# Kernel tuning notes

Hardware: AMD Instinct MI355X
Metric: run time of the kernel (lower is better)

Reference implementation:

```python
import jax, jax.numpy as jnp
import numpy as np

E = 512      # embed_dim
H = 8        # num_heads
D = E // H   # head_dim = 64
R = 32       # rot_dims (partial rotary)
THETA = 10000.0


def _rope(x):
    # x: [B, H, S, D]; rotate first R dims (interleaved pairs, lucidrains-style)
    S = x.shape[-2]
    inv_freq = THETA ** (-jnp.arange(0, R, 2, dtype=jnp.float32) / R)  # [R/2]
    ang = jnp.arange(S, dtype=jnp.float32)[:, None] * inv_freq          # [S, R/2]
    c, s = jnp.cos(ang), jnp.sin(ang)
    xr, xp = x[..., :R], x[..., R:]
    x1, x2 = xr[..., 0::2], xr[..., 1::2]
    rot = jnp.stack([x1 * c - x2 * s, x1 * s + x2 * c], axis=-1).reshape(xr.shape)
    return jnp.concatenate([rot, xp], axis=-1)


def setup_inputs() -> dict:
    key = jax.random.key(0)
    k1, k2, k3, k4 = jax.random.split(key, 4)
    B, S = 4, 2048
    x = jax.random.normal(k1, (B, S, E), dtype=jnp.float32)
    input_mask = jax.random.randint(k2, (B, S), 0, 2).astype(bool)
    W_in = jax.random.normal(k3, (3 * E, E), dtype=jnp.float32) / np.sqrt(E).astype(np.float32)
    W_out = jax.random.normal(k4, (E, E), dtype=jnp.float32) / np.sqrt(E).astype(np.float32)
    return {"x": x, "input_mask": input_mask, "W_in": W_in, "W_out": W_out}


def reference(x, input_mask, W_in, W_out):
    B, S, _ = x.shape
    # fused QKV projection (Linear, no bias): x @ W_in.T -> [B,S,3E]
    qkv = (x @ W_in.T).reshape(B, S, 3, H, D).transpose(2, 0, 3, 1, 4)  # [3,B,H,S,D]
    q, k, v = qkv[0], qkv[1], qkv[2]
    q = _rope(q)
    k = _rope(k)
    # mask: causal AND (both tokens valid OR diagonal)
    causal = jnp.tril(jnp.ones((S, S), dtype=bool))
    inv = ~input_mask                                  # [B,S]
    cross = inv[:, None, :] | inv[:, :, None]          # [B,S,S]
    square = (~cross) | jnp.eye(S, dtype=bool)         # diagonal forced True
    full = causal[None, :, :] & square                 # [B,S,S]
    scores = jnp.einsum('bhsd,bhtd->bhst', q, k) / np.float32(np.sqrt(D))
    scores = jnp.where(full[:, None, :, :], scores, -jnp.inf)
    probs = jax.nn.softmax(scores, axis=-1)
    attn = jnp.einsum('bhst,bhtd->bhsd', probs, v)
    attn = attn.transpose(0, 2, 1, 3).reshape(B, S, E)
    return attn @ W_out.T
```

## Files before the change

kernel.cpp:

```cpp
#include <hip/hip_runtime.h>
#include <math.h>

#define B_ 4
#define S_ 2048
#define E_ 512
#define H_ 8
#define D_ 64

typedef short bf16x8 __attribute__((ext_vector_type(8)));
typedef float f32x4 __attribute__((ext_vector_type(4)));

__device__ inline short f2bf(float f) {
  union { float f; unsigned u; } v; v.f = f;
  unsigned r = v.u + 0x7FFF + ((v.u >> 16) & 1);
  return (short)(r >> 16);
}
__device__ inline short f2bf_fast(float f) {
  union { float f; unsigned u; } v; v.f = f;
  return (short)((v.u + 0x8000u) >> 16);
}
__device__ inline float bf2f(short s) {
  union { unsigned u; float f; } v; v.u = ((unsigned)(unsigned short)s) << 16;
  return v.f;
}

__global__ __launch_bounds__(256) void cvt_all(
    const float* __restrict__ x, const float* __restrict__ win,
    const float* __restrict__ wout, short* __restrict__ xb,
    short* __restrict__ winb, short* __restrict__ woutb) {
  int bid = blockIdx.x;
  const float* src; short* dst; int i;
  if (bid < 4096)      { src = x;    dst = xb;    i = bid * 256 + threadIdx.x; }
  else if (bid < 4864) { src = win;  dst = winb;  i = (bid - 4096) * 256 + threadIdx.x; }
  else                 { src = wout; dst = woutb; i = (bid - 4864) * 256 + threadIdx.x; }
  float4 f = ((const float4*)src)[i];
  short4 o;
  o.x = f2bf(f.x); o.y = f2bf(f.y); o.z = f2bf(f.z); o.w = f2bf(f.w);
  ((short4*)dst)[i] = o;
}

__global__ __launch_bounds__(256) void gemm_qkv_mfma(
    const short* __restrict__ Xb,
    const short* __restrict__ Wb,
    short* __restrict__ qb, short* __restrict__ kb, short* __restrict__ vbT) {
  __shared__ __align__(16) short As[128][40];
  __shared__ __align__(16) short Bs[64][40];
  const int tid = threadIdx.x;
  const int w = tid >> 6, lane = tid & 63;
  const int l15 = lane & 15, quad = lane >> 4;
  const int wm = w & 1, wn = w >> 1;
  const int m0 = blockIdx.x * 128;
  const int n0 = blockIdx.y * 64;
  f32x4 acc[4][2];
  for (int mt = 0; mt < 4; ++mt)
    for (int nt = 0; nt < 2; ++nt) acc[mt][nt] = (f32x4){0.f, 0.f, 0.f, 0.f};

  for (int k0 = 0; k0 < E_; k0 += 32) {
    __syncthreads();
    for (int l = 0; l < 2; ++l) {
      int c = tid + 256 * l;
      int row = c >> 2, k8 = (c & 3) * 8;
      *(bf16x8*)&As[row][k8] = *(const bf16x8*)&Xb[(size_t)(m0 + row) * E_ + k0 + k8];
    }
    {
      int row = tid >> 2, k8 = (tid & 3) * 8;
      *(bf16x8*)&Bs[row][k8] = *(const bf16x8*)&Wb[(size_t)(n0 + row) * E_ + k0 + k8];
    }
    __syncthreads();
    bf16x8 a[4], bfr[2];
    for (int mt = 0; mt < 4; ++mt)
      a[mt] = *(const bf16x8*)&As[wm * 64 + mt * 16 + l15][quad * 8];
    for (int nt = 0; nt < 2; ++nt)
      bfr[nt] = *(const bf16x8*)&Bs[wn * 32 + nt * 16 + l15][quad * 8];
    for (int mt = 0; mt < 4; ++mt)
      for (int nt = 0; nt < 2; ++nt)
        acc[mt][nt] = __builtin_amdgcn_mfma_f32_16x16x32_bf16(a[mt], bfr[nt], acc[mt][nt], 0, 0, 0);
  }
  const int t3 = n0 >> 9;
  for (int nt = 0; nt < 2; ++nt) {
    const int n = n0 + wn * 32 + nt * 16 + l15;
    const int h = (n >> 6) & 7;
    const int d = n & 63;
    const bool dorope = (t3 < 2) && (d < 32);
    const float sgn = (d & 1) ? 1.f : -1.f;
    const float fr = dorope ? powf(10000.f, -(float)(2 * (d >> 1)) * (1.f / 32.f)) : 0.f;
    for (int mt = 0; mt < 4; ++mt) {
      for (int i = 0; i < 4; ++i) {
        const int m = m0 + wm * 64 + mt * 16 + quad * 4 + i;
        const int b = m >> 11, s = m & (S_ - 1);
        float val = acc[mt][nt][i];
        float pv = __shfl_xor(val, 1, 64);
        float outv = val;
        if (dorope) {
          float ang = (float)s * fr;
          float sn, cs;
          sincosf(ang, &sn, &cs);
          outv = val * cs + pv * sgn * sn;
        }
        if (t3 == 2)
          vbT[((size_t)(b * 8 + h) * D_ + d) * S_ + s] = f2bf(outv);
        else {
          short* dst = (t3 == 0) ? qb : kb;
          dst[(((size_t)(b * 8 + h)) * S_ + s) * D_ + d] = f2bf(outv);
        }
      }
    }
  }
}

__global__ __launch_bounds__(256) void gemm_out_mfma(
    const short* __restrict__ Ab, const short* __restrict__ Wb,
    float* __restrict__ out) {
  __shared__ __align__(16) short As[128][40];
  __shared__ __align__(16) short Bs[64][40];
  const int tid = threadIdx.x;
  const int w = tid >> 6, lane = tid & 63;
  const int l15 = lane & 15, quad = lane >> 4;
  const int wm = w & 1, wn = w >> 1;
  const int m0 = blockIdx.x * 128;
  const int n0 = blockIdx.y * 64;
  f32x4 acc[4][2];
  for (int mt = 0; mt < 4; ++mt)
    for (int nt = 0; nt < 2; ++nt) acc[mt][nt] = (f32x4){0.f, 0.f, 0.f, 0.f};

  for (int k0 = 0; k0 < E_; k0 += 32) {
    __syncthreads();
    for (int l = 0; l < 2; ++l) {
      int c = tid + 256 * l;
      int row = c >> 2, k8 = (c & 3) * 8;
      *(bf16x8*)&As[row][k8] = *(const bf16x8*)&Ab[(size_t)(m0 + row) * E_ + k0 + k8];
    }
    {
      int row = tid >> 2, k8 = (tid & 3) * 8;
      *(bf16x8*)&Bs[row][k8] = *(const bf16x8*)&Wb[(size_t)(n0 + row) * E_ + k0 + k8];
    }
    __syncthreads();
    bf16x8 a[4], bfr[2];
    for (int mt = 0; mt < 4; ++mt)
      a[mt] = *(const bf16x8*)&As[wm * 64 + mt * 16 + l15][quad * 8];
    for (int nt = 0; nt < 2; ++nt)
      bfr[nt] = *(const bf16x8*)&Bs[wn * 32 + nt * 16 + l15][quad * 8];
    for (int mt = 0; mt < 4; ++mt)
      for (int nt = 0; nt < 2; ++nt)
        acc[mt][nt] = __builtin_amdgcn_mfma_f32_16x16x32_bf16(a[mt], bfr[nt], acc[mt][nt], 0, 0, 0);
  }
  for (int mt = 0; mt < 4; ++mt)
    for (int nt = 0; nt < 2; ++nt) {
      const int n = n0 + wn * 32 + nt * 16 + l15;
      for (int i = 0; i < 4; ++i) {
        const int m = m0 + wm * 64 + mt * 16 + quad * 4 + i;
        out[(size_t)m * E_ + n] = acc[mt][nt][i];
      }
    }
}

__global__ __launch_bounds__(256) void flash_mfma(
    const short* __restrict__ qb, const short* __restrict__ kb,
    const short* __restrict__ vbT, const int* __restrict__ maskp,
    short* __restrict__ pb0, short* __restrict__ pb1,
    float* __restrict__ lb0, float* __restrict__ lb1,
    short* __restrict__ ob) {
  __shared__ __align__(16) short Ks[64][72];
  __shared__ __align__(16) short VT[64][72];
  __shared__ __align__(16) short Pl[4][16][72];
  __shared__ float kbias[64];
  const int tid = threadIdx.x;
  const int w = tid >> 6, lane = tid & 63;
  const int l15 = lane & 15, quad = lane >> 4;
  const int bid = blockIdx.x;
  const int u = bid & 7, v = bid >> 3;
  const int bh = (u << 2) | (v & 3);
  const int w2 = v >> 2;
  const int pair = w2 & 15;
  const int kh = w2 >> 4;
  const int b = bh >> 3, hd = bh & 7;
  const short* qbase = qb + (size_t)bh * S_ * D_;
  const short* kbase = kb + (size_t)bh * S_ * D_;
  const short* vtb   = vbT + (size_t)bh * D_ * S_;
  short* PB = kh ? pb1 : pb0;
  float* LB = kh ? lb1 : lb0;
  const float c2 = 0.1803368801f;
  bf16x8 ones;
  for (int j = 0; j < 8; ++j) ones[j] = (short)0x3F80;

  for (int seg = 0; seg < 2; ++seg) {
    const int qt = (seg == 0) ? pair : 31 - pair;
    const int r0 = qt * 64;
    const int mid = (qt + 2) >> 1;
    const int lo = kh ? mid : 0;
    const int hi = kh ? (qt + 1) : mid;
    bf16x8 aq[2];
    {
      const short* qrow = qbase + (size_t)(r0 + 16 * w + l15) * D_;
      aq[0] = *(const bf16x8*)&qrow[quad * 8];
      aq[1] = *(const bf16x8*)&qrow[32 + quad * 8];
    }
    f32x4 o[4], lsum;
    for (int no = 0; no < 4; ++no) o[no] = (f32x4){0.f, 0.f, 0.f, 0.f};
    lsum = (f32x4){0.f, 0.f, 0.f, 0.f};

    for (int kt = lo; kt < hi; ++kt) {
      const int t0 = kt * 64;
      __syncthreads();
      for (int l = 0; l < 2; ++l) {
        int idx = tid + 256 * l;
        int row = idx >> 3, ch = (idx & 7) * 8;
        *(bf16x8*)&Ks[row][ch] = *(const bf16x8*)(kbase + (size_t)(t0 + row) * D_ + ch);
        *(bf16x8*)&VT[row][ch] = *(const bf16x8*)(vtb + (size_t)row * S_ + t0 + ch);
      }
      if (tid < 64)
        kbias[tid] = maskp[b * S_ + t0 + tid] ? -23.08312f : -1.0e38f;
      __syncthreads();
      f32x4 sfr[4];
      for (int nb = 0; nb < 4; ++nb) sfr[nb] = (f32x4){0.f, 0.f, 0.f, 0.f};
      for (int nb = 0; nb < 4; ++nb)
        for (int ks = 0; ks < 2; ++ks) {
          bf16x8 bk = *(const bf16x8*)&Ks[l15 + 16 * nb][32 * ks + quad * 8];
          sfr[nb] = __builtin_amdgcn_mfma_f32_16x16x32_bf16(aq[ks], bk, sfr[nb], 0, 0, 0);
        }
      if (kt < qt) {
        for (int nb = 0; nb < 4; ++nb) {
          const float bb = kbias[l15 + 16 * nb];
          for (int i = 0; i < 4; ++i)
            Pl[w][quad * 4 + i][l15 + 16 * nb] = f2bf_fast(exp2f(sfr[nb][i] * c2 + bb));
        }
      } else {
        for (int nb = 0; nb < 4; ++nb) {
          const int tg = l15 + 16 * nb;
          const float bb = kbias[l15 + 16 * nb];
          for (int i = 0; i < 4; ++i) {
            const float bbi = (tg > 16 * w + quad * 4 + i) ? -1.0e38f : bb;
            Pl[w][quad * 4 + i][l15 + 16 * nb] = f2bf_fast(exp2f(sfr[nb][i] * c2 + bbi));
          }
        }
      }
      asm volatile("s_waitcnt lgkmcnt(0)" ::: "memory");
      bf16x8 ap0 = *(const bf16x8*)&Pl[w][l15][quad * 8];
      bf16x8 ap1 = *(const bf16x8*)&Pl[w][l15][32 + quad * 8];
      for (int no = 0; no < 4; ++no) {
        bf16x8 bv0 = *(const bf16x8*)&VT[16 * no + l15][quad * 8];
        bf16x8 bv1 = *(const bf16x8*)&VT[16 * no + l15][32 + quad * 8];
        o[no] = __builtin_amdgcn_mfma_f32_16x16x32_bf16(ap0, bv0, o[no], 0, 0, 0);
        o[no] = __builtin_amdgcn_mfma_f32_16x16x32_bf16(ap1, bv1, o[no], 0, 0, 0);
      }
      lsum = __builtin_amdgcn_mfma_f32_16x16x32_bf16(ap0, ones, lsum, 0, 0, 0);
      lsum = __builtin_amdgcn_mfma_f32_16x16x32_bf16(ap1, ones, lsum, 0, 0, 0);
    }
    for (int i = 0; i < 4; ++i) {
      const int s = r0 + 16 * w + quad * 4 + i;
      const int qm = maskp[b * S_ + s];
      const size_t row = (size_t)(b * S_ + s) * E_ + hd * D_;
      if (kh == 0 && !qm) {
        for (int no = 0; no < 4; ++no) {
          const int d = l15 + 16 * no;
          ob[row + d] = vtb[(size_t)d * S_ + s];
        }
      }
      for (int no = 0; no < 4; ++no)
        PB[row + l15 + 16 * no] = f2bf(o[no][i]);
      if (l15 == 0)
        LB[bh * S_ + s] = lsum[i];
    }
  }
}

__global__ __launch_bounds__(256) void merge_kernel(
    const short* __restrict__ pb0, const short* __restrict__ pb1,
    const float* __restrict__ lb0, const float* __restrict__ lb1,
    const int* __restrict__ maskp, short* __restrict__ ob) {
  int idx = blockIdx.x * 256 + threadIdx.x;
  int m = idx >> 6, e = (idx & 63) * 8;
  if (!maskp[m]) return;
  int b = m >> 11, s = m & (S_ - 1);
  int bh = b * 8 + (e >> 6);
  float l = lb0[bh * S_ + s] + lb1[bh * S_ + s];
  float inv = 1.f / l;
  bf16x8 p0 = *(const bf16x8*)&pb0[(size_t)m * E_ + e];
  bf16x8 p1 = *(const bf16x8*)&pb1[(size_t)m * E_ + e];
  bf16x8 r;
  for (int j = 0; j < 8; ++j)
    r[j] = f2bf((bf2f(p0[j]) + bf2f(p1[j])) * inv);
  *(bf16x8*)&ob[(size_t)m * E_ + e] = r;
}

extern "C" void kernel_launch(void* const* d_in, const int* in_sizes, int n_in,
                              void* d_out, int out_size, void* d_ws, size_t ws_size,
                              hipStream_t stream) {
  const float* x    = (const float*)d_in[0];
  const int*   mask = (const int*)d_in[1];
  const float* Win  = (const float*)d_in[2];
  const float* Wout = (const float*)d_in[3];
  float* out = (float*)d_out;

  short* Xb    = (short*)d_ws;
  short* Winb  = Xb + 8192 * 512;
  short* Woutb = Winb + 1536 * 512;
  short* qb    = Woutb + 512 * 512;
  short* kb    = qb + 32 * 2048 * 64;
  short* vbT   = kb + 32 * 2048 * 64;
  short* ob    = vbT + 32 * 2048 * 64;
  short* pb0   = ob + 8192 * 512;
  short* pb1   = pb0 + 8192 * 512;
  float* lb0   = (float*)(pb1 + 8192 * 512);
  float* lb1   = lb0 + 32 * 2048;

  cvt_all<<<5120, 256, 0, stream>>>(x, Win, Wout, Xb, Winb, Woutb);
  gemm_qkv_mfma<<<dim3(64, 24), 256, 0, stream>>>(Xb, Winb, qb, kb, vbT);
  flash_mfma<<<1024, 256, 0, stream>>>(qb, kb, vbT, mask, pb0, pb1, lb0, lb1, ob);
  merge_kernel<<<2048, 256, 0, stream>>>(pb0, pb1, lb0, lb1, mask, ob);
  gemm_out_mfma<<<dim3(64, 8), 256, 0, stream>>>(ob, Woutb, out);
}
```

Measured before the change: 169.9 us.

## Use direct global-to-LDS loads and 128x128 tiles in QKV GEMM

Both projection GEMMs now stage their A and B tiles with global_load_lds. This writes global data straight into shared memory instead of passing it through registers, and it drops the padded LDS layout. The QKV GEMM also widens its N tile from 64 to 128, so each wave holds a 4x4 MFMA accumulator grid and the grid has half as many blocks. The RoPE frequency now comes from exp2f instead of powf. Removing the row padding may add LDS bank conflicts on fragment reads, and the larger tile raises register pressure.

```diff
diff --git a/kernel.cpp b/kernel.cpp
--- a/kernel.cpp
+++ b/kernel.cpp
@@ -22,6 +22,12 @@
 __device__ inline float bf2f(short s) {
   union { unsigned u; float f; } v; v.u = ((unsigned)(unsigned short)s) << 16;
   return v.f;
+}
+
+__device__ __forceinline__ void gload16(const short* g, short* l) {
+  __builtin_amdgcn_global_load_lds(
+      (__attribute__((address_space(1))) void*)g,
+      (__attribute__((address_space(3))) void*)l, 16, 0, 0);
 }
 
 __global__ __launch_bounds__(256) void cvt_all(
@@ -43,47 +49,59 @@
     const short* __restrict__ Xb,
     const short* __restrict__ Wb,
     short* __restrict__ qb, short* __restrict__ kb, short* __restrict__ vbT) {
-  __shared__ __align__(16) short As[128][40];
-  __shared__ __align__(16) short Bs[64][40];
+  __shared__ __align__(16) short As[128 * 32];
+  __shared__ __align__(16) short Bs[128 * 32];
   const int tid = threadIdx.x;
   const int w = tid >> 6, lane = tid & 63;
   const int l15 = lane & 15, quad = lane >> 4;
   const int wm = w & 1, wn = w >> 1;
   const int m0 = blockIdx.x * 128;
-  const int n0 = blockIdx.y * 64;
-  f32x4 acc[4][2];
+  const int n0 = blockIdx.y * 128;
+
+  const int srow = tid >> 2, sch = (tid & 3) * 8;
+  const short* gA0 = Xb + (size_t)(m0 + srow) * E_ + sch;
+  const short* gA1 = Xb + (size_t)(m0 + srow + 64) * E_ + sch;
+  const short* gB0 = Wb + (size_t)(n0 + srow) * E_ + sch;
+  const short* gB1 = Wb + (size_t)(n0 + srow + 64) * E_ + sch;
+  short* lA0 = &As[tid * 8];
+  short* lA1 = &As[tid * 8 + 2048];
+  short* lB0 = &Bs[tid * 8];
+  short* lB1 = &Bs[tid * 8 + 2048];
+
+  f32x4 acc[4][4];
   for (int mt = 0; mt < 4; ++mt)
-    for (int nt = 0; nt < 2; ++nt) acc[mt][nt] = (f32x4){0.f, 0.f, 0.f, 0.f};
+    for (int nt = 0; nt < 4; ++nt) acc[mt][nt] = (f32x4){0.f, 0.f, 0.f, 0.f};
 
   for (int k0 = 0; k0 < E_; k0 += 32) {
     __syncthreads();
-    for (int l = 0; l < 2; ++l) {
-      int c = tid + 256 * l;
-      int row = c >> 2, k8 = (c & 3) * 8;
-      *(bf16x8*)&As[row][k8] = *(const bf16x8*)&Xb[(size_t)(m0 + row) * E_ + k0 + k8];
-    }
-    {
-      int row = tid >> 2, k8 = (tid & 3) * 8;
-      *(bf16x8*)&Bs[row][k8] = *(const bf16x8*)&Wb[(size_t)(n0 + row) * E_ + k0 + k8];
-    }
+    gload16(gA0, lA0);
+    gload16(gA1, lA1);
+    gload16(gB0, lB0);
+    gload16(gB1, lB1);
+    gA0 += 32; gA1 += 32; gB0 += 32; gB1 += 32;
     __syncthreads();
-    bf16x8 a[4], bfr[2];
+    bf16x8 a[4], bfr[4];
+#pragma unroll
     for (int mt = 0; mt < 4; ++mt)
-      a[mt] = *(const bf16x8*)&As[wm * 64 + mt * 16 + l15][quad * 8];
-    for (int nt = 0; nt < 2; ++nt)
-      bfr[nt] = *(const bf16x8*)&Bs[wn * 32 + nt * 16 + l15][quad * 8];
+      a[mt] = *(const bf16x8*)&As[(wm * 64 + mt * 16 + l15) * 32 + quad * 8];
+#pragma unroll
+    for (int nt = 0; nt < 4; ++nt)
+      bfr[nt] = *(const bf16x8*)&Bs[(wn * 64 + nt * 16 + l15) * 32 + quad * 8];
+#pragma unroll
     for (int mt = 0; mt < 4; ++mt)
-      for (int nt = 0; nt < 2; ++nt)
+#pragma unroll
+      for (int nt = 0; nt < 4; ++nt)
         acc[mt][nt] = __builtin_amdgcn_mfma_f32_16x16x32_bf16(a[mt], bfr[nt], acc[mt][nt], 0, 0, 0);
   }
+
   const int t3 = n0 >> 9;
-  for (int nt = 0; nt < 2; ++nt) {
-    const int n = n0 + wn * 32 + nt * 16 + l15;
+  for (int nt = 0; nt < 4; ++nt) {
+    const int n = n0 + wn * 64 + nt * 16 + l15;
     const int h = (n >> 6) & 7;
     const int d = n & 63;
     const bool dorope = (t3 < 2) && (d < 32);
     const float sgn = (d & 1) ? 1.f : -1.f;
-    const float fr = dorope ? powf(10000.f, -(float)(2 * (d >> 1)) * (1.f / 32.f)) : 0.f;
+    const float fr = dorope ? exp2f((float)(d >> 1) * -0.8304820237f) : 0.f;
     for (int mt = 0; mt < 4; ++mt) {
       for (int i = 0; i < 4; ++i) {
         const int m = m0 + wm * 64 + mt * 16 + quad * 4 + i;
@@ -111,36 +129,44 @@
 __global__ __launch_bounds__(256) void gemm_out_mfma(
     const short* __restrict__ Ab, const short* __restrict__ Wb,
     float* __restrict__ out) {
-  __shared__ __align__(16) short As[128][40];
-  __shared__ __align__(16) short Bs[64][40];
+  __shared__ __align__(16) short As[128 * 32];
+  __shared__ __align__(16) short Bs[64 * 32];
   const int tid = threadIdx.x;
   const int w = tid >> 6, lane = tid & 63;
   const int l15 = lane & 15, quad = lane >> 4;
   const int wm = w & 1, wn = w >> 1;
   const int m0 = blockIdx.x * 128;
   const int n0 = blockIdx.y * 64;
+
+  const int srow = tid >> 2, sch = (tid & 3) * 8;
+  const short* gA0 = Ab + (size_t)(m0 + srow) * E_ + sch;
+  const short* gA1 = Ab + (size_t)(m0 + srow + 64) * E_ + sch;
+  const short* gB0 = Wb + (size_t)(n0 + srow) * E_ + sch;
+  short* lA0 = &As[tid * 8];
+  short* lA1 = &As[tid * 8 + 2048];
+  short* lB0 = &Bs[tid * 8];
+
   f32x4 acc[4][2];
   for (int mt = 0; mt < 4; ++mt)
     for (int nt = 0; nt < 2; ++nt) acc[mt][nt] = (f32x4){0.f, 0.f, 0.f, 0.f};
 
   for (int k0 = 0; k0 < E_; k0 += 32) {
     __syncthreads();
-    for (int l = 0; l < 2; ++l) {
-      int c = tid + 256 * l;
-      int row = c >> 2, k8 = (c & 3) * 8;
-      *(bf16x8*)&As[row][k8] = *(const bf16x8*)&Ab[(size_t)(m0 + row) * E_ + k0 + k8];
-    }
-    {
-      int row = tid >> 2, k8 = (tid & 3) * 8;
-      *(bf16x8*)&Bs[row][k8] = *(const bf16x8*)&Wb[(size_t)(n0 + row) * E_ + k0 + k8];
-    }
+    gload16(gA0, lA0);
+    gload16(gA1, lA1);
+    gload16(gB0, lB0);
+    gA0 += 32; gA1 += 32; gB0 += 32;
     __syncthreads();
     bf16x8 a[4], bfr[2];
+#pragma unroll
     for (int mt = 0; mt < 4; ++mt)
-      a[mt] = *(const bf16x8*)&As[wm * 64 + mt * 16 + l15][quad * 8];
+      a[mt] = *(const bf16x8*)&As[(wm * 64 + mt * 16 + l15) * 32 + quad * 8];
+#pragma unroll
     for (int nt = 0; nt < 2; ++nt)
-      bfr[nt] = *(const bf16x8*)&Bs[wn * 32 + nt * 16 + l15][quad * 8];
+      bfr[nt] = *(const bf16x8*)&Bs[(wn * 32 + nt * 16 + l15) * 32 + quad * 8];
+#pragma unroll
     for (int mt = 0; mt < 4; ++mt)
+#pragma unroll
       for (int nt = 0; nt < 2; ++nt)
         acc[mt][nt] = __builtin_amdgcn_mfma_f32_16x16x32_bf16(a[mt], bfr[nt], acc[mt][nt], 0, 0, 0);
   }
@@ -305,7 +331,7 @@
   float* lb1   = lb0 + 32 * 2048;
 
   cvt_all<<<5120, 256, 0, stream>>>(x, Win, Wout, Xb, Winb, Woutb);
-  gemm_qkv_mfma<<<dim3(64, 24), 256, 0, stream>>>(Xb, Winb, qb, kb, vbT);
+  gemm_qkv_mfma<<<dim3(64, 12), 256, 0, stream>>>(Xb, Winb, qb, kb, vbT);
   flash_mfma<<<1024, 256, 0, stream>>>(qb, kb, vbT, mask, pb0, pb1, lb0, lb1, ob);
   merge_kernel<<<2048, 256, 0, stream>>>(pb0, pb1, lb0, lb1, mask, ob);
   gemm_out_mfma<<<dim3(64, 8), 256, 0, stream>>>(ob, Woutb, out);
```

Result: no change. 167.4 us (-1.5%).
